# Kernel optimization log

Measured on AMD Instinct MI355X. Metric: run time of the kernel, lower is better.

## Reference

```python
import jax, jax.numpy as jnp
import numpy as np

B, P, NT, NX = 16, 8, 512, 2048


def setup_inputs() -> dict:
    key = jax.random.key(0)
    k1, k2 = jax.random.split(key)
    # sorted breakpoints on [0, 1]: 0, interior (sorted), 1  -> [B, P+1]
    interior = jnp.sort(jax.random.uniform(k1, (B, P - 1)), axis=1)
    xs = jnp.concatenate([jnp.zeros((B, 1)), interior, jnp.ones((B, 1))], axis=1)
    ks = jax.random.uniform(k2, (B, P))                 # densities in (0,1)
    pieces_mask = jnp.ones((B, P), dtype=jnp.int32)     # all pieces valid
    dx = jnp.full((B,), 1.0 / NX, dtype=jnp.float32)
    dt = jnp.full((B,), 0.5 / NX, dtype=jnp.float32)    # CFL: dt <= dx (max|f'|=1)
    t_coords = jnp.zeros((B, 1, NT, NX), dtype=jnp.float32)  # only shape is used
    return dict(xs=xs, ks=ks, pieces_mask=pieces_mask, dx=dx, dt=dt, t_coords=t_coords)


def _godunov_flux(uL, uR):
    # Greenshield flux f(u) = u*(1-u), concave with max f(0.5)=0.25.
    f = lambda u: u * (1.0 - u)
    fL, fR = f(uL), f(uR)
    # uL <= uR: min over [uL,uR] attained at an endpoint (concave f)
    fmin = jnp.minimum(fL, fR)
    # uL >  uR: max over [uR,uL]; = 0.25 if sonic point 0.5 inside interval
    fmax = jnp.where((uL >= 0.5) & (uR <= 0.5), 0.25, jnp.maximum(fL, fR))
    return jnp.where(uL <= uR, fmin, fmax)


def reference(xs, ks, pieces_mask, dx, dt, t_coords):
    nt, nx = t_coords.shape[2], t_coords.shape[3]
    dx_v, dt_v = dx[0], dt[0]
    # --- discretize piecewise-constant ICs (vectorized over batch) ---
    n_pieces = jnp.sum(pieces_mask, axis=1)                       # [B]
    # right boundary of each piece; invalid pieces pushed to +inf
    bnds = jnp.where(pieces_mask.astype(bool), xs[:, 1:], jnp.inf)  # [B, P]
    xc = (jnp.arange(nx, dtype=xs.dtype) + 0.5) * dx_v            # cell centers [nx]
    idx = jnp.sum(xc[None, None, :] >= bnds[:, :, None], axis=1)  # [B, nx]
    idx = jnp.minimum(idx, n_pieces[:, None] - 1)
    ic = jnp.take_along_axis(ks, idx, axis=1)                     # [B, nx]
    # --- Godunov time marching with 'ic' ghost cells (1 cell each side) ---
    gL, gR = ic[:, :1], ic[:, -1:]
    lam = dt_v / dx_v

    def step(u, _):
        ue = jnp.concatenate([gL, u, gR], axis=1)                 # [B, nx+2]
        F = _godunov_flux(ue[:, :-1], ue[:, 1:])                  # [B, nx+1]
        u_new = u - lam * (F[:, 1:] - F[:, :-1])
        return u_new, u_new

    _, rest = jax.lax.scan(step, ic, None, length=nt - 1)         # [nt-1, B, nx]
    sol = jnp.concatenate([ic[None], rest], axis=0)               # [nt, B, nx]
    sol = jnp.transpose(sol, (1, 0, 2))                           # [B, nt, nx]
    return sol[:, None]                                           # [B, 1, nt, nx]
```

## Files before the change

kernel.cpp:

```cpp
#include <hip/hip_runtime.h>

namespace {

constexpr int kB  = 16;
constexpr int kP  = 8;
constexpr int kNT = 512;
constexpr int kNX = 2048;
constexpr int kW  = 48;
constexpr int kOwn = 32;
constexpr int kNS = 11;
constexpr int kCpB = 64;
constexpr int kSolver = kB * kCpB;

constexpr size_t kHaloBytes = (size_t)kNS * kB * kNX * 4;
constexpr int    kPoison    = -1;

typedef float v2f __attribute__((ext_vector_type(2)));

__device__ __forceinline__ float dpp_shr1(float x) {
    return __builtin_bit_cast(float,
        __builtin_amdgcn_update_dpp(0, __builtin_bit_cast(int, x), 0x138, 0xF, 0xF, true));
}
__device__ __forceinline__ float dpp_shl1(float x) {
    return __builtin_bit_cast(float,
        __builtin_amdgcn_update_dpp(0, __builtin_bit_cast(int, x), 0x130, 0xF, 0xF, true));
}

__device__ __forceinline__ float max3n(float xL, float xR) {
    float m;
    asm("v_max3_f32 %0, -%1, %2, 0" : "=v"(m) : "v"(xL), "v"(xR));
    return m;
}

__device__ __forceinline__ void mall_store(int* p, float v) {
    (void)__hip_atomic_exchange(p, __builtin_bit_cast(int, v),
                                __ATOMIC_RELAXED, __HIP_MEMORY_SCOPE_AGENT);
}
__device__ __forceinline__ int mall_loadi(const int* p) {
    return __hip_atomic_load(p, __ATOMIC_RELAXED, __HIP_MEMORY_SCOPE_AGENT);
}

__global__ __launch_bounds__(64)
void godunov_fused(const float* __restrict__ xs,
                   const float* __restrict__ ks,
                   const int*   __restrict__ pm,
                   const float* __restrict__ dxp,
                   const float* __restrict__ dtp,
                   float* __restrict__ out,
                   int*   __restrict__ halo)
{
    const int p    = blockIdx.x;
    const int b    = p >> 6;
    const int k    = p & 63;
    const int lane = threadIdx.x;
    const int rs   = k * kOwn - kW;
    const int gi0  = rs + 2 * lane;

    const float dxv = dxp[0];
    const float lam = dtp[0] / dxv;
    const v2f  h2   = {0.5f, 0.5f};

    int np = 0;
    float bnds[kP];
#pragma unroll
    for (int j = 0; j < kP; ++j) {
        int m = pm[b * kP + j];
        np += m;
        bnds[j] = m ? xs[b * (kP + 1) + j + 1] : __builtin_inff();
    }
    const int cap = np - 1;

    auto icval = [&](int gi) -> float {
        float xc = ((float)gi + 0.5f) * dxv;
        int idx = 0;
#pragma unroll
        for (int j = 0; j < kP; ++j) idx += (xc >= bnds[j]) ? 1 : 0;
        idx = min(idx, cap);
        return ks[b * kP + idx];
    };

    const float gL = icval(0);
    const float gR = icval(kNX - 1);

    const bool  laneIn  = (gi0 >= 0) && (gi0 < kNX);
    const float gvv     = (gi0 < 0) ? gL : gR;
    const float gxv     = gvv - 0.5f;
    const bool  edgeBlk = (k < 2) || (k >= kCpB - 2);

    float x0 = (laneIn ? icval(gi0)     : gvv) - 0.5f;
    float x1 = (laneIn ? icval(gi0 + 1) : gvv) - 0.5f;

    const bool writer = (lane >= 24) && (lane < 40);

    if (writer) {
        float* p0 = out + ((size_t)b * kNT) * kNX;
        *reinterpret_cast<float2*>(p0 + gi0) = make_float2(x0 + 0.5f, x1 + 0.5f);
    }

    char* pstore = writer
        ? (char*)(out + ((size_t)b * kNT + 1) * kNX + gi0)
        : (char*)(halo + p * kOwn + 2 * (lane & 15));
    const size_t incB = writer ? (size_t)kNX * sizeof(float) : 0;

    auto step_store = [&]() {
        float xm = dpp_shr1(x1);
        float xp = dpp_shl1(x0);
        float m0 = max3n(xm, x0);
        float m1 = max3n(x0, x1);
        float m2 = max3n(x1, xp);
        v2f mA = {m0, m1};
        v2f GA = mA * mA;
        float G2 = m2 * m2;
        float t0 = __builtin_fmaf( lam, GA.y, x0);
        x0       = __builtin_fmaf(-lam, GA.x, t0);
        float t1 = __builtin_fmaf(-lam, GA.y, x1);
        x1       = __builtin_fmaf( lam, G2,   t1);
        if (edgeBlk) {
            x0 = laneIn ? x0 : gxv;
            x1 = laneIn ? x1 : gxv;
        }
        v2f xv = {x0, x1};
        v2f sv = xv + h2;
        *reinterpret_cast<float2*>(pstore) = make_float2(sv.x, sv.y);
        pstore += incB;
    };

#pragma unroll 1
    for (int s = 0; s < kNS; ++s) {
        if (s > 0) {
            const int* slot = halo + ((size_t)s * kB + b) * kNX;
            if (lane < 24) {
                if (gi0 >= 0) {
                    const int* hp = slot + gi0;
                    int v0, v1;
                    for (int it = 0; it < (1 << 22); ++it) {
                        v0 = mall_loadi(hp); v1 = mall_loadi(hp + 1);
                        if (v0 != kPoison && v1 != kPoison) break;
                        __builtin_amdgcn_s_sleep(1);
                    }
                    x0 = __builtin_bit_cast(float, v0) - 0.5f;
                    x1 = __builtin_bit_cast(float, v1) - 0.5f;
                }
            } else if (lane >= 40) {
                if (gi0 < kNX) {
                    const int* hp = slot + gi0;
                    int v0, v1;
                    for (int it = 0; it < (1 << 22); ++it) {
                        v0 = mall_loadi(hp); v1 = mall_loadi(hp + 1);
                        if (v0 != kPoison && v1 != kPoison) break;
                        __builtin_amdgcn_s_sleep(1);
                    }
                    x0 = __builtin_bit_cast(float, v0) - 0.5f;
                    x1 = __builtin_bit_cast(float, v1) - 0.5f;
                }
            }
        }

        const int noct = (s == kNS - 1) ? 3 : 6;
#pragma unroll 1
        for (int g = 0; g < noct; ++g) {
#pragma unroll
            for (int q = 0; q < 8; ++q) step_store();
        }
        if (s == kNS - 1) {
#pragma unroll
            for (int q = 0; q < 7; ++q) step_store();
        }

        if (s < kNS - 1 && writer) {
            int* hp = halo + ((size_t)(s + 1) * kB + b) * kNX + gi0;
            mall_store(hp,     x0 + 0.5f);
            mall_store(hp + 1, x1 + 0.5f);
        }
    }
}

}

extern "C" void kernel_launch(void* const* d_in, const int* in_sizes, int n_in,
                              void* d_out, int out_size, void* d_ws, size_t ws_size,
                              hipStream_t stream) {
    const float* xs  = (const float*)d_in[0];
    const float* ks  = (const float*)d_in[1];
    const int*   pm  = (const int*)d_in[2];
    const float* dxv = (const float*)d_in[3];
    const float* dtv = (const float*)d_in[4];
    float* out = (float*)d_out;

    int* halo = (int*)d_ws;

    hipMemsetAsync(halo, 0xFF, kHaloBytes, stream);

    hipLaunchKernelGGL(godunov_fused, dim3(kSolver), dim3(64), 0, stream,
                       xs, ks, pm, dxv, dtv, out, halo);
}
```

Baseline: 46.86 us.

## Use one cell per lane with twice as many blocks and halo stages

Each 64-lane block now owns 16 cells with one cell per lane, down from 32 cells with two per lane. The block count doubles to 128 per batch row, the halo width drops to 24, and the stage count doubles to 22 stages of 24 steps. This spreads the work over more wavefronts and shortens the per-step dependency chain. In exchange there are twice as many cross-block halo handoffs through the spin-wait, more redundant halo compute per owned cell, and narrower stores.

```diff
diff --git a/kernel.cpp b/kernel.cpp
--- a/kernel.cpp
+++ b/kernel.cpp
@@ -6,16 +6,14 @@
 constexpr int kP  = 8;
 constexpr int kNT = 512;
 constexpr int kNX = 2048;
-constexpr int kW  = 48;
-constexpr int kOwn = 32;
-constexpr int kNS = 11;
-constexpr int kCpB = 64;
+constexpr int kW  = 24;
+constexpr int kOwn = 16;
+constexpr int kNS = 22;
+constexpr int kCpB = 128;
 constexpr int kSolver = kB * kCpB;
 
 constexpr size_t kHaloBytes = (size_t)kNS * kB * kNX * 4;
 constexpr int    kPoison    = -1;
-
-typedef float v2f __attribute__((ext_vector_type(2)));
 
 __device__ __forceinline__ float dpp_shr1(float x) {
     return __builtin_bit_cast(float,
@@ -50,15 +48,14 @@
                    int*   __restrict__ halo)
 {
     const int p    = blockIdx.x;
-    const int b    = p >> 6;
-    const int k    = p & 63;
+    const int b    = p >> 7;
+    const int k    = p & 127;
     const int lane = threadIdx.x;
     const int rs   = k * kOwn - kW;
-    const int gi0  = rs + 2 * lane;
+    const int gi   = rs + lane;
 
     const float dxv = dxp[0];
     const float lam = dtp[0] / dxv;
-    const v2f  h2   = {0.5f, 0.5f};
 
     int np = 0;
     float bnds[kP];
@@ -70,8 +67,8 @@
     }
     const int cap = np - 1;
 
-    auto icval = [&](int gi) -> float {
-        float xc = ((float)gi + 0.5f) * dxv;
+    auto icval = [&](int g) -> float {
+        float xc = ((float)g + 0.5f) * dxv;
         int idx = 0;
 #pragma unroll
         for (int j = 0; j < kP; ++j) idx += (xc >= bnds[j]) ? 1 : 0;
@@ -82,46 +79,37 @@
     const float gL = icval(0);
     const float gR = icval(kNX - 1);
 
-    const bool  laneIn  = (gi0 >= 0) && (gi0 < kNX);
-    const float gvv     = (gi0 < 0) ? gL : gR;
+    const bool  laneIn  = (gi >= 0) && (gi < kNX);
+    const float gvv     = (gi < 0) ? gL : gR;
     const float gxv     = gvv - 0.5f;
     const bool  edgeBlk = (k < 2) || (k >= kCpB - 2);
 
-    float x0 = (laneIn ? icval(gi0)     : gvv) - 0.5f;
-    float x1 = (laneIn ? icval(gi0 + 1) : gvv) - 0.5f;
+    float x = (laneIn ? icval(gi) : gvv) - 0.5f;
 
     const bool writer = (lane >= 24) && (lane < 40);
 
     if (writer) {
-        float* p0 = out + ((size_t)b * kNT) * kNX;
-        *reinterpret_cast<float2*>(p0 + gi0) = make_float2(x0 + 0.5f, x1 + 0.5f);
+        out[((size_t)b * kNT) * kNX + gi] = x + 0.5f;
     }
 
     char* pstore = writer
-        ? (char*)(out + ((size_t)b * kNT + 1) * kNX + gi0)
-        : (char*)(halo + p * kOwn + 2 * (lane & 15));
+        ? (char*)(out + ((size_t)b * kNT + 1) * kNX + gi)
+        : (char*)(halo + (size_t)p * kOwn + (lane & 15));
     const size_t incB = writer ? (size_t)kNX * sizeof(float) : 0;
 
     auto step_store = [&]() {
-        float xm = dpp_shr1(x1);
-        float xp = dpp_shl1(x0);
-        float m0 = max3n(xm, x0);
-        float m1 = max3n(x0, x1);
-        float m2 = max3n(x1, xp);
-        v2f mA = {m0, m1};
-        v2f GA = mA * mA;
-        float G2 = m2 * m2;
-        float t0 = __builtin_fmaf( lam, GA.y, x0);
-        x0       = __builtin_fmaf(-lam, GA.x, t0);
-        float t1 = __builtin_fmaf(-lam, GA.y, x1);
-        x1       = __builtin_fmaf( lam, G2,   t1);
+        float xm = dpp_shr1(x);
+        float xp = dpp_shl1(x);
+        float m0 = max3n(xm, x);
+        float m1 = max3n(x, xp);
+        float G0 = m0 * m0;
+        float G1 = m1 * m1;
+        float t  = __builtin_fmaf( lam, G1, x);
+        x        = __builtin_fmaf(-lam, G0, t);
         if (edgeBlk) {
-            x0 = laneIn ? x0 : gxv;
-            x1 = laneIn ? x1 : gxv;
+            x = laneIn ? x : gxv;
         }
-        v2f xv = {x0, x1};
-        v2f sv = xv + h2;
-        *reinterpret_cast<float2*>(pstore) = make_float2(sv.x, sv.y);
+        *reinterpret_cast<float*>(pstore) = x + 0.5f;
         pstore += incB;
     };
 
@@ -130,47 +118,44 @@
         if (s > 0) {
             const int* slot = halo + ((size_t)s * kB + b) * kNX;
             if (lane < 24) {
-                if (gi0 >= 0) {
-                    const int* hp = slot + gi0;
-                    int v0, v1;
+                if (gi >= 0) {
+                    const int* hp = slot + gi;
+                    int v;
                     for (int it = 0; it < (1 << 22); ++it) {
-                        v0 = mall_loadi(hp); v1 = mall_loadi(hp + 1);
-                        if (v0 != kPoison && v1 != kPoison) break;
+                        v = mall_loadi(hp);
+                        if (v != kPoison) break;
                         __builtin_amdgcn_s_sleep(1);
                     }
-                    x0 = __builtin_bit_cast(float, v0) - 0.5f;
-                    x1 = __builtin_bit_cast(float, v1) - 0.5f;
+                    x = __builtin_bit_cast(float, v) - 0.5f;
                 }
             } else if (lane >= 40) {
-                if (gi0 < kNX) {
-                    const int* hp = slot + gi0;
-                    int v0, v1;
+                if (gi < kNX) {
+                    const int* hp = slot + gi;
+                    int v;
                     for (int it = 0; it < (1 << 22); ++it) {
-                        v0 = mall_loadi(hp); v1 = mall_loadi(hp + 1);
-                        if (v0 != kPoison && v1 != kPoison) break;
+                        v = mall_loadi(hp);
+                        if (v != kPoison) break;
                         __builtin_amdgcn_s_sleep(1);
                     }
-                    x0 = __builtin_bit_cast(float, v0) - 0.5f;
-                    x1 = __builtin_bit_cast(float, v1) - 0.5f;
+                    x = __builtin_bit_cast(float, v) - 0.5f;
                 }
             }
         }
 
-        const int noct = (s == kNS - 1) ? 3 : 6;
+        if (s < kNS - 1) {
 #pragma unroll 1
-        for (int g = 0; g < noct; ++g) {
+            for (int g = 0; g < 3; ++g) {
 #pragma unroll
-            for (int q = 0; q < 8; ++q) step_store();
-        }
-        if (s == kNS - 1) {
+                for (int q = 0; q < 8; ++q) step_store();
+            }
+        } else {
 #pragma unroll
             for (int q = 0; q < 7; ++q) step_store();
         }
 
         if (s < kNS - 1 && writer) {
-            int* hp = halo + ((size_t)(s + 1) * kB + b) * kNX + gi0;
-            mall_store(hp,     x0 + 0.5f);
-            mall_store(hp + 1, x1 + 0.5f);
+            int* hp = halo + ((size_t)(s + 1) * kB + b) * kNX + gi;
+            mall_store(hp, x + 0.5f);
         }
     }
 }
```

Result: slower. 80.27 us (+71.3%).
